# Kernel optimization log

Measured on AMD Instinct MI355X. Metric: run time of the kernel, lower is better.

Reference implementation:

```python
import jax, jax.numpy as jnp
import numpy as np

N = 100000
E = 1600000
IN_DIM = 128
HID_DIM = 128
NUM_CLASSES = 40


def setup_inputs() -> dict:
    key = jax.random.key(0)
    k1, k2, k3, k4, k5, k6 = jax.random.split(key, 6)
    x = jax.random.normal(k1, (N, IN_DIM), dtype=jnp.float32)
    e = jax.random.randint(k2, (2, E), 0, N, dtype=jnp.int64)
    s1 = 1.0 / np.sqrt(IN_DIM)
    s2 = 1.0 / np.sqrt(HID_DIM)
    W1 = jax.random.uniform(k3, (IN_DIM, HID_DIM), jnp.float32, -s1, s1)
    b1 = jax.random.uniform(k4, (HID_DIM,), jnp.float32, -s1, s1)
    W2 = jax.random.uniform(k5, (HID_DIM, NUM_CLASSES), jnp.float32, -s2, s2)
    b2 = jax.random.uniform(k6, (NUM_CLASSES,), jnp.float32, -s2, s2)
    return {"x": x, "e": e, "W1": W1, "b1": b1, "W2": W2, "b2": b2}


def _gcn_conv(x, src, dst, norm, W, b, n):
    # linear transform first (PyG GCNConv), then normalized aggregation
    h = x @ W                                    # [N, d_out]
    out = jax.ops.segment_sum(h[src] * norm[:, None], dst, num_segments=n)
    return out + b


def reference(x, e, W1, b1, W2, b2):
    n = x.shape[0]
    loop = jnp.arange(n, dtype=e.dtype)
    src = jnp.concatenate([e[0], loop])          # add self-loops
    dst = jnp.concatenate([e[1], loop])
    deg = jax.ops.segment_sum(jnp.ones_like(dst, dtype=x.dtype), dst, num_segments=n)
    d_inv_sqrt = deg ** -0.5                     # deg >= 1 due to self-loops
    norm = d_inv_sqrt[src] * d_inv_sqrt[dst]     # symmetric normalization
    h = jax.nn.relu(_gcn_conv(x, src, dst, norm, W1, b1, n))
    return _gcn_conv(h, src, dst, norm, W2, b2, n)
```

## Files before the change

### kernel.cpp

```cpp
#include <hip/hip_runtime.h>


typedef unsigned int u32;
typedef unsigned short u16;
typedef __attribute__((ext_vector_type(8))) short short8;
typedef __attribute__((ext_vector_type(4))) float floatx4;

#define CHUNK 4096

#define REP7(M)  M(0) M(1) M(2) M(3) M(4) M(5) M(6)
#define REP8(M)  M(0) M(1) M(2) M(3) M(4) M(5) M(6) M(7)

static __device__ inline u16 f2bf(float f) {
    u32 u = __float_as_uint(f);
    return (u16)((u + 0x7FFFu + ((u >> 16) & 1u)) >> 16);
}
static __device__ inline u32 pack2(float a, float b) {
    return (u32)f2bf(a) | ((u32)f2bf(b) << 16);
}
static __device__ inline float bflo(u32 u) { return __uint_as_float(u << 16); }
static __device__ inline float bfhi(u32 u) { return __uint_as_float(u & 0xffff0000u); }

static __device__ inline bool detect_is64(const int* e32, int lane) {
    bool nz = e32[2 * lane + 1] != 0;
    return __ballot(nz) == 0ull;
}

__global__ void k_prepW(const float* __restrict__ W1, const float* __restrict__ W2,
                        u16* __restrict__ WTb, u16* __restrict__ W2Tb) {
    int id = blockIdx.x * 256 + threadIdx.x;
    if (id < 16384) {
        int k = id >> 7, c = id & 127;
        WTb[c * 128 + k] = f2bf(W1[id]);
    } else {
        int id2 = id - 16384;
        if (id2 < 6144) {
            int c = id2 >> 7, k = id2 & 127;
            W2Tb[id2] = f2bf(c < 40 ? W2[k * 40 + c] : 0.f);
        }
    }
}

__global__ __launch_bounds__(256) void k_front(const void* __restrict__ e_raw,
                                               int E, int NC, int NB,
                                               int* __restrict__ histG,
                                               const float* __restrict__ X,
                                               const u16* __restrict__ WTb,
                                               u16* __restrict__ H1s, int n) {
    __shared__ u32 smem[64 * 68 + 128 * 68];
    const int tid = threadIdx.x;
    if ((int)blockIdx.x < NC) {
        int* h = (int*)smem;
        h[tid] = 0; h[tid + 256] = 0;
        __syncthreads();
        const int* e32 = (const int*)e_raw;
        bool is64 = detect_is64(e32, tid & 63);
        int c = blockIdx.x;
        int j0 = c * CHUNK, j1 = min(E, j0 + CHUNK);
        for (int j = j0 + tid; j < j1; j += 256) {
            int d = is64 ? (int)((const long long*)e_raw)[E + j] : e32[E + j];
            atomicAdd(&h[d >> 8], 1);
        }
        __syncthreads();
        for (int b = tid; b < NB; b += 256) histG[(size_t)b * NC + c] = h[b];
        return;
    }
    u32* As = smem;
    u32* Bs = smem + 64 * 68;
    const int row0 = ((int)blockIdx.x - NC) * 64;
#pragma unroll
    for (int it = 0; it < 8; it++) {
        int i = tid + it * 256;
        int r = i >> 5;
        int c4 = (i & 31) << 2;
        int gr = row0 + r;
        float4 v = make_float4(0.f, 0.f, 0.f, 0.f);
        if (gr < n) v = *(const float4*)(X + (size_t)gr * 128 + c4);
        uint2 p;
        p.x = pack2(v.x, v.y);
        p.y = pack2(v.z, v.w);
        *(uint2*)&As[r * 68 + (c4 >> 1)] = p;
    }
#pragma unroll
    for (int it = 0; it < 8; it++) {
        int i = tid + it * 256;
        int r = i >> 4;
        int c4 = (i & 15) << 2;
        *(uint4*)&Bs[r * 68 + c4] =
            *(const uint4*)((const u32*)WTb + (size_t)r * 64 + c4);
    }
    __syncthreads();

    const int lane = tid & 63;
    const int wave = tid >> 6;
    const int wr = wave >> 1;
    const int wc = wave & 1;
    const int mrow = lane & 15;
    const int quad = lane >> 4;

    floatx4 acc[2][4] = {};
    for (int k0 = 0; k0 < 128; k0 += 32) {
        int koff = (k0 >> 1) + quad * 4;
        short8 a[2], b[4];
#pragma unroll
        for (int i = 0; i < 2; i++)
            a[i] = *(const short8*)&As[((wr * 2 + i) * 16 + mrow) * 68 + koff];
#pragma unroll
        for (int j = 0; j < 4; j++)
            b[j] = *(const short8*)&Bs[((wc * 4 + j) * 16 + mrow) * 68 + koff];
#pragma unroll
        for (int i = 0; i < 2; i++)
#pragma unroll
            for (int j = 0; j < 4; j++)
                acc[i][j] = __builtin_amdgcn_mfma_f32_16x16x32_bf16(
                    a[i], b[j], acc[i][j], 0, 0, 0);
    }
#pragma unroll
    for (int i = 0; i < 2; i++) {
        int gr0 = row0 + (wr * 2 + i) * 16 + quad * 4;
#pragma unroll
        for (int j = 0; j < 4; j++) {
            int gcol = (wc * 4 + j) * 16 + mrow;
#pragma unroll
            for (int rg = 0; rg < 4; rg++) {
                int grow = gr0 + rg;
                if (grow < n)
                    H1s[(size_t)grow * 128 + gcol] = f2bf(acc[i][j][rg]);
            }
        }
    }
}

__global__ void k_scan1(const int* __restrict__ in, int* __restrict__ out,
                        int* __restrict__ bsum, int n) {
    __shared__ int sh[256];
    int i = blockIdx.x * 256 + threadIdx.x;
    int v = (i < n) ? in[i] : 0;
    sh[threadIdx.x] = v;
    __syncthreads();
    for (int off = 1; off < 256; off <<= 1) {
        int t = (threadIdx.x >= off) ? sh[threadIdx.x - off] : 0;
        __syncthreads();
        sh[threadIdx.x] += t;
        __syncthreads();
    }
    if (i < n) out[i] = sh[threadIdx.x] - v;
    if (threadIdx.x == 255) bsum[blockIdx.x] = sh[255];
}

static __device__ inline void scan_bsum_local(const int* __restrict__ bsum,
                                              int nb, int* bs, int* sct,
                                              int t) {
    int carry = 0;
    for (int base = 0; base < nb; base += 256) {
        int v = (base + t < nb) ? bsum[base + t] : 0;
        sct[t] = v;
        __syncthreads();
        for (int off = 1; off < 256; off <<= 1) {
            int u = (t >= off) ? sct[t - off] : 0;
            __syncthreads();
            sct[t] += u;
            __syncthreads();
        }
        if (base + t < nb) bs[base + t] = carry + sct[t] - v;
        carry += sct[255];
        __syncthreads();
    }
}

__global__ __launch_bounds__(256) void k_place(const void* __restrict__ e_raw,
                                               const int* __restrict__ histOff,
                                               const int* __restrict__ bsum,
                                               u32* __restrict__ tmp,
                                               int E, int NB, int NC, int nbH) {
    __shared__ int cur[512];
    __shared__ int bs[1024];
    __shared__ int sct[256];
    int c = blockIdx.x;
    int t = threadIdx.x;
    scan_bsum_local(bsum, nbH, bs, sct, t);
    for (int b = t; b < NB; b += 256) {
        int idx = b * NC + c;
        cur[b] = histOff[idx] + bs[idx >> 8];
    }
    __syncthreads();
    const int* e32 = (const int*)e_raw;
    bool is64 = detect_is64(e32, t & 63);
    int j0 = c * CHUNK, j1 = min(E, j0 + CHUNK);
    for (int j = j0 + t; j < j1; j += 256) {
        int s, d;
        if (is64) {
            s = (int)((const long long*)e_raw)[j];
            d = (int)((const long long*)e_raw)[E + j];
        } else {
            s = e32[j];
            d = e32[E + j];
        }
        int pos = atomicAdd(&cur[d >> 8], 1);
        tmp[pos] = (u32)s | ((u32)(d & 255) << 24);
    }
}

__global__ __launch_bounds__(256) void k_degsort(const u32* __restrict__ tmp,
                                                 const int* __restrict__ histOff,
                                                 const int* __restrict__ bsum,
                                                 int* __restrict__ degI,
                                                 float* __restrict__ dinv,
                                                 int* __restrict__ rs,
                                                 int* __restrict__ eSrc,
                                                 int n, int NB, int NC, int E,
                                                 int nbH) {
    __shared__ int cnt[256];
    __shared__ int sh[256];
    __shared__ int cur[256];
    __shared__ int bs[1024];
    int b = blockIdx.x;
    int t = threadIdx.x;
    scan_bsum_local(bsum, nbH, bs, sh, t);
    cnt[t] = 0;
    __syncthreads();
    int i0 = b * NC;
    int seg0 = histOff[i0] + bs[i0 >> 8];
    int seg1 = E;
    if (b + 1 < NB) {
        int i1 = (b + 1) * NC;
        seg1 = histOff[i1] + bs[i1 >> 8];
    }
    for (int j = seg0 + t; j < seg1; j += 256) atomicAdd(&cnt[tmp[j] >> 24], 1);
    __syncthreads();
    int v = cnt[t];
    sh[t] = v;
    __syncthreads();
    for (int off = 1; off < 256; off <<= 1) {
        int u = (t >= off) ? sh[t - off] : 0;
        __syncthreads();
        sh[t] += u;
        __syncthreads();
    }
    int myStart = seg0 + sh[t] - v;
    cur[t] = myStart;
    int node = b * 256 + t;
    if (node < n) {
        degI[node] = v;
        dinv[node] = rsqrtf((float)v + 1.0f);
        rs[node] = myStart;
    }
    __syncthreads();
    for (int j = seg0 + t; j < seg1; j += 256) {
        u32 rec = tmp[j];
        int dl = rec >> 24;
        int s = (int)(rec & 0x00FFFFFFu);
        int pos = atomicAdd(&cur[dl], 1);
        eSrc[pos] = s;
    }
}

__global__ __launch_bounds__(256) void k_gather128(
    const uint4* __restrict__ Hb4, const int* __restrict__ rs,
    const int* __restrict__ degI, const int* __restrict__ eSrc,
    const float* __restrict__ dinv, const float* __restrict__ b1,
    uint4* __restrict__ outb4, int n) {
    const int wave = threadIdx.x >> 6;
    const int lane = threadIdx.x & 63;
    const int q = lane >> 4;
    const int m = lane & 15;
    const int node = blockIdx.x * 4 + wave;
    if (node >= n) return;
    const int start = rs[node];
    const int deg = degI[node];
    float a0 = 0.f, a1 = 0.f, a2 = 0.f, a3 = 0.f;
    float a4 = 0.f, a5 = 0.f, a6 = 0.f, a7 = 0.f;

#define GACC(U, W)                                                    \
    a0 = fmaf(W, bflo(U.x), a0); a1 = fmaf(W, bfhi(U.x), a1);         \
    a2 = fmaf(W, bflo(U.y), a2); a3 = fmaf(W, bfhi(U.y), a3);         \
    a4 = fmaf(W, bflo(U.z), a4); a5 = fmaf(W, bfhi(U.z), a5);         \
    a6 = fmaf(W, bflo(U.w), a6); a7 = fmaf(W, bfhi(U.w), a7);

    for (int base = 0; base < deg; base += 64) {
        int mS = 0;
        float mW = 0.f;
        if (base + lane < deg) { mS = eSrc[start + base + lane]; mW = dinv[mS]; }
        int cnt = min(64, deg - base);
        int t = 0;
        for (; t + 16 <= cnt; t += 16) {
            int s0 = __shfl(mS, t + q),      s1 = __shfl(mS, t + 4 + q);
            int s2 = __shfl(mS, t + 8 + q),  s3 = __shfl(mS, t + 12 + q);
            float w0 = __shfl(mW, t + q),     w1 = __shfl(mW, t + 4 + q);
            float w2 = __shfl(mW, t + 8 + q), w3 = __shfl(mW, t + 12 + q);
            uint4 u0 = Hb4[(size_t)s0 * 16 + m];
            uint4 u1 = Hb4[(size_t)s1 * 16 + m];
            uint4 u2 = Hb4[(size_t)s2 * 16 + m];
            uint4 u3 = Hb4[(size_t)s3 * 16 + m];
            GACC(u0, w0)
            GACC(u1, w1)
            GACC(u2, w2)
            GACC(u3, w3)
        }
        for (; t < cnt; t += 4) {
            int idx = t + q;
            int s = __shfl(mS, idx);
            float w = __shfl(mW, idx);
            uint4 u = Hb4[(size_t)s * 16 + m];
            GACC(u, w)
        }
    }
#undef GACC
#define GRED(v) v += __shfl_xor(v, 16); v += __shfl_xor(v, 32);
    GRED(a0) GRED(a1) GRED(a2) GRED(a3) GRED(a4) GRED(a5) GRED(a6) GRED(a7)
#undef GRED
    if (q == 0) {
        const float di = dinv[node];
        uint4 us = Hb4[(size_t)node * 16 + m];
        float4 bva = ((const float4*)b1)[m * 2];
        float4 bvb = ((const float4*)b1)[m * 2 + 1];
        float i0 = fmaf(di, bflo(us.x), a0), i1 = fmaf(di, bfhi(us.x), a1);
        float i2 = fmaf(di, bflo(us.y), a2), i3 = fmaf(di, bfhi(us.y), a3);
        float i4 = fmaf(di, bflo(us.z), a4), i5 = fmaf(di, bfhi(us.z), a5);
        float i6 = fmaf(di, bflo(us.w), a6), i7 = fmaf(di, bfhi(us.w), a7);
        float r0 = fmaxf(fmaf(di, i0, bva.x), 0.f);
        float r1 = fmaxf(fmaf(di, i1, bva.y), 0.f);
        float r2 = fmaxf(fmaf(di, i2, bva.z), 0.f);
        float r3 = fmaxf(fmaf(di, i3, bva.w), 0.f);
        float r4 = fmaxf(fmaf(di, i4, bvb.x), 0.f);
        float r5 = fmaxf(fmaf(di, i5, bvb.y), 0.f);
        float r6 = fmaxf(fmaf(di, i6, bvb.z), 0.f);
        float r7 = fmaxf(fmaf(di, i7, bvb.w), 0.f);
        uint4 o;
        o.x = pack2(r0, r1);
        o.y = pack2(r2, r3);
        o.z = pack2(r4, r5);
        o.w = pack2(r6, r7);
        outb4[(size_t)node * 16 + m] = o;
    }
}

__global__ __launch_bounds__(256) void k_gemm2(const u32* __restrict__ A1b,
                                               const u16* __restrict__ W2Tb,
                                               const float* __restrict__ dinv,
                                               u16* __restrict__ H2s, int n) {
    __shared__ u32 As[64 * 68];
    __shared__ u32 Bs[48 * 68];
    const int tid = threadIdx.x;
    const int row0 = blockIdx.x * 64;
#pragma unroll
    for (int it = 0; it < 4; it++) {
        int i = tid + it * 256;
        int r = i >> 4;
        int c4 = (i & 15) << 2;
        int gr = row0 + r;
        uint4 v = make_uint4(0u, 0u, 0u, 0u);
        if (gr < n) v = *(const uint4*)(A1b + (size_t)gr * 64 + c4);
        *(uint4*)&As[r * 68 + c4] = v;
    }
#pragma unroll
    for (int it = 0; it < 3; it++) {
        int i = tid + it * 256;
        int r = i >> 4;
        int c4 = (i & 15) << 2;
        *(uint4*)&Bs[r * 68 + c4] =
            *(const uint4*)((const u32*)W2Tb + (size_t)r * 64 + c4);
    }
    __syncthreads();

    const int lane = tid & 63;
    const int wave = tid >> 6;
    const int mrow = lane & 15;
    const int quad = lane >> 4;

    floatx4 acc[3] = {};
    for (int k0 = 0; k0 < 128; k0 += 32) {
        int koff = (k0 >> 1) + quad * 4;
        short8 a = *(const short8*)&As[(wave * 16 + mrow) * 68 + koff];
#pragma unroll
        for (int j = 0; j < 3; j++) {
            short8 b = *(const short8*)&Bs[(j * 16 + mrow) * 68 + koff];
            acc[j] = __builtin_amdgcn_mfma_f32_16x16x32_bf16(a, b, acc[j], 0, 0, 0);
        }
    }
    int gr0 = row0 + wave * 16 + quad * 4;
    float dv[4];
#pragma unroll
    for (int rg = 0; rg < 4; rg++)
        dv[rg] = (gr0 + rg < n) ? dinv[gr0 + rg] : 0.f;
#pragma unroll
    for (int j = 0; j < 3; j++) {
        int gcol = j * 16 + mrow;
        if (gcol < 40) {
            int sl = (gcol >= 20) ? 1 : 0;
            int c = gcol - sl * 20;
            u16* dstp = H2s + (size_t)sl * ((size_t)n * 20);
#pragma unroll
            for (int rg = 0; rg < 4; rg++) {
                int grow = gr0 + rg;
                if (grow < n)
                    dstp[(size_t)grow * 20 + c] = f2bf(dv[rg] * acc[j][rg]);
            }
        }
    }
}

__global__ __launch_bounds__(256) void k_gather40(
    const u32* __restrict__ H2b, const int* __restrict__ rs,
    const int* __restrict__ degI, const int* __restrict__ eSrc,
    const float* __restrict__ dinv, const float* __restrict__ b2,
    float* __restrict__ out, int n) {
    const int lane = threadIdx.x & 63;
    const int wave = threadIdx.x >> 6;
    const int g = lane / 10;
    const int l = lane - g * 10;
    const int slice = blockIdx.x & 1;
    const int chunk = blockIdx.x >> 1;
    if (g >= 6) return;
    const u32* __restrict__ Hs = H2b + (size_t)slice * ((size_t)n * 10);

    const int node = chunk * 24 + wave * 6 + g;
    if (node >= n) return;
    const int start = rs[node];
    const int deg = degI[node];
    float ax = 0.f, ay = 0.f;
    u32 r0, r1, r2, r3, r4, r5, r6, r7;
    u32 u0, u1, u2, u3, u4, u5, u6, u7;
    int t = 0;

#define PH(K) u##K = Hs[(size_t)r##K * 10 + l];
#define PF(K) r##K = (u32)eSrc[bq + K];
#define PA(K) ax += bflo(u##K); ay += bfhi(u##K);

    if (deg >= 8) {
        int bq = start;
        REP8(PF)
        for (; t + 16 <= deg; t += 8) {
            REP8(PH)
            bq = start + t + 8;
            REP8(PF)
            REP8(PA)
        }
        REP8(PH)
        REP8(PA)
        t += 8;
    }
    if (t < deg) {
        const int bq = start + t;
        const int rm = deg - t - 1;
#define PTF(K) r##K = (u32)eSrc[bq + min(K, rm)];
#define PTA(K) if (K <= rm) { ax += bflo(u##K); ay += bfhi(u##K); }
        REP7(PTF)
        REP7(PH)
        REP7(PTA)
#undef PTF
#undef PTA
    }
#undef PH
#undef PF
#undef PA
    const float di = dinv[node];
    const u32 us = Hs[(size_t)node * 10 + l];
    const float2 bv = *(const float2*)(b2 + (slice * 10 + l) * 2);
    float ox = fmaf(di, ax + bflo(us), bv.x);
    float oy = fmaf(di, ay + bfhi(us), bv.y);
    *(float2*)(out + (size_t)node * 40 + (slice * 10 + l) * 2) =
        make_float2(ox, oy);
}

extern "C" void kernel_launch(void* const* d_in, const int* in_sizes, int n_in,
                              void* d_out, int out_size, void* d_ws, size_t ws_size,
                              hipStream_t stream) {
    const float* x  = (const float*)d_in[0];
    const void*  e  = d_in[1];
    const float* W1 = (const float*)d_in[2];
    const float* b1 = (const float*)d_in[3];
    const float* W2 = (const float*)d_in[4];
    const float* b2 = (const float*)d_in[5];
    float* out = (float*)d_out;

    const int n = in_sizes[0] / 128;
    const int E = in_sizes[1] / 2;
    const int NB = (n + 255) / 256;
    const int NC = (E + CHUNK - 1) / CHUNK;
    const int NH = NB * NC;
    const int nbH = (NH + 255) / 256;
    const int G1 = (n + 63) / 64;

    int*   degI    = (int*)d_ws;
    int*   rs      = degI + n;
    int*   bsumH   = rs + n;
    float* dinv    = (float*)(bsumH + 1024);
    int*   histG   = (int*)(dinv + n);
    int*   histOff = histG + NH;
    size_t off = (size_t)((char*)(histOff + NH) - (char*)d_ws);
    off = (off + 15) & ~(size_t)15;
    u16*   WTb    = (u16*)((char*)d_ws + off);
    u16*   W2Tb   = WTb + 16384;
    off = (size_t)((char*)(W2Tb + 6144) - (char*)d_ws);
    off = (off + 15) & ~(size_t)15;
    u32*   tmp    = (u32*)((char*)d_ws + off);
    int*   eSrc   = (int*)(tmp + (size_t)E);
    u16*   H1s    = (u16*)(eSrc + (size_t)E);
    uint4* H1q    = (uint4*)H1s;
    u32*   A1b    = (u32*)(H1s + (size_t)n * 128);
    uint4* A1q    = (uint4*)A1b;
    u16*   H2s    = (u16*)(A1b + (size_t)n * 64);
    u32*   H2b    = (u32*)H2s;

    k_prepW<<<88, 256, 0, stream>>>(W1, W2, WTb, W2Tb);
    k_front<<<NC + G1, 256, 0, stream>>>(e, E, NC, NB, histG, x, WTb, H1s, n);

    k_scan1<<<nbH, 256, 0, stream>>>(histG, histOff, bsumH, NH);
    k_place<<<NC, 256, 0, stream>>>(e, histOff, bsumH, tmp, E, NB, NC, nbH);

    k_degsort<<<NB, 256, 0, stream>>>(tmp, histOff, bsumH, degI, dinv, rs,
                                      eSrc, n, NB, NC, E, nbH);

    k_gather128<<<(n + 3) / 4, 256, 0, stream>>>(H1q, rs, degI, eSrc, dinv,
                                                 b1, A1q, n);
    k_gemm2<<<(n + 63) / 64, 256, 0, stream>>>(A1b, W2Tb, dinv, H2s, n);
    k_gather40<<<2 * ((n + 23) / 24), 256, 0, stream>>>(H2b, rs, degI, eSrc,
                                                        dinv, b2, out, n);
}
```

Baseline: 300.6 us.

## Fold weight bf16 transpose into GEMM kernels and halve edge chunk size

Removes the separate weight-preparation kernel. Each GEMM block now loads fp32 W1/W2 directly and converts and transposes them into shared memory itself. The edge chunk size is halved, which doubles the histogram column count, so the block-sum buffers are enlarged to match. This saves one launch and gives more parallel blocks in the histogram/place stages, at the cost of redundant per-block weight conversion with scattered 16-bit LDS stores and larger scans.

```diff
diff --git a/kernel.cpp b/kernel.cpp
--- a/kernel.cpp
+++ b/kernel.cpp
@@ -6,7 +6,7 @@
 typedef __attribute__((ext_vector_type(8))) short short8;
 typedef __attribute__((ext_vector_type(4))) float floatx4;
 
-#define CHUNK 4096
+#define CHUNK 2048
 
 #define REP7(M)  M(0) M(1) M(2) M(3) M(4) M(5) M(6)
 #define REP8(M)  M(0) M(1) M(2) M(3) M(4) M(5) M(6) M(7)
@@ -24,28 +24,13 @@
 static __device__ inline bool detect_is64(const int* e32, int lane) {
     bool nz = e32[2 * lane + 1] != 0;
     return __ballot(nz) == 0ull;
-}
-
-__global__ void k_prepW(const float* __restrict__ W1, const float* __restrict__ W2,
-                        u16* __restrict__ WTb, u16* __restrict__ W2Tb) {
-    int id = blockIdx.x * 256 + threadIdx.x;
-    if (id < 16384) {
-        int k = id >> 7, c = id & 127;
-        WTb[c * 128 + k] = f2bf(W1[id]);
-    } else {
-        int id2 = id - 16384;
-        if (id2 < 6144) {
-            int c = id2 >> 7, k = id2 & 127;
-            W2Tb[id2] = f2bf(c < 40 ? W2[k * 40 + c] : 0.f);
-        }
-    }
 }
 
 __global__ __launch_bounds__(256) void k_front(const void* __restrict__ e_raw,
                                                int E, int NC, int NB,
                                                int* __restrict__ histG,
                                                const float* __restrict__ X,
-                                               const u16* __restrict__ WTb,
+                                               const float* __restrict__ W1,
                                                u16* __restrict__ H1s, int n) {
     __shared__ u32 smem[64 * 68 + 128 * 68];
     const int tid = threadIdx.x;
@@ -81,13 +66,19 @@
         p.y = pack2(v.z, v.w);
         *(uint2*)&As[r * 68 + (c4 >> 1)] = p;
     }
-#pragma unroll
-    for (int it = 0; it < 8; it++) {
-        int i = tid + it * 256;
-        int r = i >> 4;
-        int c4 = (i & 15) << 2;
-        *(uint4*)&Bs[r * 68 + c4] =
-            *(const uint4*)((const u32*)WTb + (size_t)r * 64 + c4);
+    {
+        u16* B16 = (u16*)Bs;
+#pragma unroll
+        for (int it = 0; it < 16; it++) {
+            int i = tid + it * 256;
+            int k = i >> 5;
+            int c4 = (i & 31) << 2;
+            float4 v = *(const float4*)(W1 + k * 128 + c4);
+            B16[(c4 + 0) * 136 + k] = f2bf(v.x);
+            B16[(c4 + 1) * 136 + k] = f2bf(v.y);
+            B16[(c4 + 2) * 136 + k] = f2bf(v.z);
+            B16[(c4 + 3) * 136 + k] = f2bf(v.w);
+        }
     }
     __syncthreads();
 
@@ -174,7 +165,7 @@
                                                u32* __restrict__ tmp,
                                                int E, int NB, int NC, int nbH) {
     __shared__ int cur[512];
-    __shared__ int bs[1024];
+    __shared__ int bs[2048];
     __shared__ int sct[256];
     int c = blockIdx.x;
     int t = threadIdx.x;
@@ -213,7 +204,7 @@
     __shared__ int cnt[256];
     __shared__ int sh[256];
     __shared__ int cur[256];
-    __shared__ int bs[1024];
+    __shared__ int bs[2048];
     int b = blockIdx.x;
     int t = threadIdx.x;
     scan_bsum_local(bsum, nbH, bs, sh, t);
@@ -336,7 +327,7 @@
 }
 
 __global__ __launch_bounds__(256) void k_gemm2(const u32* __restrict__ A1b,
-                                               const u16* __restrict__ W2Tb,
+                                               const float* __restrict__ W2,
                                                const float* __restrict__ dinv,
                                                u16* __restrict__ H2s, int n) {
     __shared__ u32 As[64 * 68];
@@ -353,13 +344,22 @@
         if (gr < n) v = *(const uint4*)(A1b + (size_t)gr * 64 + c4);
         *(uint4*)&As[r * 68 + c4] = v;
     }
-#pragma unroll
-    for (int it = 0; it < 3; it++) {
-        int i = tid + it * 256;
-        int r = i >> 4;
-        int c4 = (i & 15) << 2;
-        *(uint4*)&Bs[r * 68 + c4] =
-            *(const uint4*)((const u32*)W2Tb + (size_t)r * 64 + c4);
+    for (int i = tid; i < 8 * 68; i += 256) Bs[40 * 68 + i] = 0;
+    {
+        u16* B16 = (u16*)Bs;
+#pragma unroll
+        for (int it = 0; it < 5; it++) {
+            int i = tid + it * 256;
+            if (i < 1280) {
+                int k = i / 10;
+                int c4 = (i - k * 10) * 4;
+                float4 v = *(const float4*)(W2 + k * 40 + c4);
+                B16[(c4 + 0) * 136 + k] = f2bf(v.x);
+                B16[(c4 + 1) * 136 + k] = f2bf(v.y);
+                B16[(c4 + 2) * 136 + k] = f2bf(v.z);
+                B16[(c4 + 3) * 136 + k] = f2bf(v.w);
+            }
+        }
     }
     __syncthreads();
 
@@ -485,14 +485,10 @@
     int*   degI    = (int*)d_ws;
     int*   rs      = degI + n;
     int*   bsumH   = rs + n;
-    float* dinv    = (float*)(bsumH + 1024);
+    float* dinv    = (float*)(bsumH + 2048);
     int*   histG   = (int*)(dinv + n);
     int*   histOff = histG + NH;
     size_t off = (size_t)((char*)(histOff + NH) - (char*)d_ws);
-    off = (off + 15) & ~(size_t)15;
-    u16*   WTb    = (u16*)((char*)d_ws + off);
-    u16*   W2Tb   = WTb + 16384;
-    off = (size_t)((char*)(W2Tb + 6144) - (char*)d_ws);
     off = (off + 15) & ~(size_t)15;
     u32*   tmp    = (u32*)((char*)d_ws + off);
     int*   eSrc   = (int*)(tmp + (size_t)E);
@@ -503,8 +499,7 @@
     u16*   H2s    = (u16*)(A1b + (size_t)n * 64);
     u32*   H2b    = (u32*)H2s;
 
-    k_prepW<<<88, 256, 0, stream>>>(W1, W2, WTb, W2Tb);
-    k_front<<<NC + G1, 256, 0, stream>>>(e, E, NC, NB, histG, x, WTb, H1s, n);
+    k_front<<<NC + G1, 256, 0, stream>>>(e, E, NC, NB, histG, x, W1, H1s, n);
 
     k_scan1<<<nbH, 256, 0, stream>>>(histG, histOff, bsumH, NH);
     k_place<<<NC, 256, 0, stream>>>(e, histOff, bsumH, tmp, E, NB, NC, nbH);
@@ -514,7 +509,7 @@
 
     k_gather128<<<(n + 3) / 4, 256, 0, stream>>>(H1q, rs, degI, eSrc, dinv,
                                                  b1, A1q, n);
-    k_gemm2<<<(n + 63) / 64, 256, 0, stream>>>(A1b, W2Tb, dinv, H2s, n);
+    k_gemm2<<<(n + 63) / 64, 256, 0, stream>>>(A1b, W2, dinv, H2s, n);
     k_gather40<<<2 * ((n + 23) / 24), 256, 0, stream>>>(H2b, rs, degI, eSrc,
                                                         dinv, b2, out, n);
 }
```

New measurement: 328.5 us. +9.3%, slower.
